# Kernel optimization log

Measured on AMD Instinct MI355X. Metric: run time of the kernel, lower is better.

Reference implementation:

```python
import jax, jax.numpy as jnp
import numpy as np

MAX_DIST = 3          # census patch radius -> 7x7 neighborhood
PATCH = 2 * MAX_DIST + 1


def _warp(img, flow):
    """Bilinear warp (Resample2d): sample img at (x + u, y + v). Coords clamped to border."""
    B, C, H, W = img.shape
    gy, gx = jnp.meshgrid(jnp.arange(H, dtype=img.dtype), jnp.arange(W, dtype=img.dtype), indexing='ij')
    x = gx[None] + flow[:, 0]           # [B,H,W]
    y = gy[None] + flow[:, 1]
    x0 = jnp.floor(x); y0 = jnp.floor(y)
    wx = x - x0; wy = y - y0            # bilinear weights
    x0i = jnp.clip(x0, 0, W - 1).astype(jnp.int32)
    x1i = jnp.clip(x0 + 1.0, 0, W - 1).astype(jnp.int32)
    y0i = jnp.clip(y0, 0, H - 1).astype(jnp.int32)
    y1i = jnp.clip(y0 + 1.0, 0, H - 1).astype(jnp.int32)

    def gather(im_b, yi, xi):           # im_b [C,H,W], yi/xi [H,W] -> [C,H,W]
        return im_b[:, yi, xi]
    g = jax.vmap(gather)
    Ia = g(img, y0i, x0i); Ib = g(img, y0i, x1i)
    Ic = g(img, y1i, x0i); Id = g(img, y1i, x1i)
    wx = wx[:, None]; wy = wy[:, None]  # [B,1,H,W]
    return Ia * (1 - wx) * (1 - wy) + Ib * wx * (1 - wy) + Ic * (1 - wx) * wy + Id * wx * wy


def _census_transform(image):
    """Ternary census transform: grayscale, extract 7x7 patches, normalized center differences."""
    gray = (0.299 * image[:, 0:1] + 0.587 * image[:, 1:2] + 0.114 * image[:, 2:3]) * 255.0
    w = jnp.eye(PATCH * PATCH, dtype=image.dtype).reshape(PATCH * PATCH, 1, PATCH, PATCH)
    patches = jax.lax.conv_general_dilated(
        gray, w, window_strides=(1, 1), padding=[(MAX_DIST, MAX_DIST)] * 2,
        dimension_numbers=('NCHW', 'OIHW', 'NCHW'))   # [B,49,H,W]
    t = patches - gray
    return t / jnp.sqrt(0.81 + t * t)


def _border_mask(B, H, W, dtype):
    m = jnp.zeros((H, W), dtype).at[MAX_DIST:H - MAX_DIST, MAX_DIST:W - MAX_DIST].set(1.0)
    return jnp.broadcast_to(m[None, None], (B, 1, H, W))


def _charbonnier(x, mask, alpha=0.45, eps=0.001):
    err = (x * x + eps * eps) ** alpha * mask
    return jnp.sum(err) / x.size


def _census_loss(im1, im2_warped, mask):
    t1 = _census_transform(im1)
    t2 = _census_transform(im2_warped)
    d = (t1 - t2) ** 2
    dist = jnp.sum(d / (0.1 + d), axis=1, keepdims=True)   # soft Hamming distance [B,1,H,W]
    B, _, H, W = dist.shape
    return _charbonnier(dist, mask * _border_mask(B, H, W, dist.dtype))


def setup_inputs() -> dict:
    key = jax.random.key(0)
    ks = jax.random.split(key, 6)
    B, H, W = 4, 320, 768
    return {
        'former': jax.random.uniform(ks[0], (B, 3, H, W), jnp.float32),
        'latter': jax.random.uniform(ks[1], (B, 3, H, W), jnp.float32),
        'disp_est_scale': jax.random.normal(ks[2], (B, 2, H, W), jnp.float32) * 3.0,
        'disp_est_scale_2': jax.random.normal(ks[3], (B, 2, H, W), jnp.float32) * 3.0,
        'fw_mask': jax.random.uniform(ks[4], (B, 1, H, W), jnp.float32),
        'bw_mask': jax.random.uniform(ks[5], (B, 1, H, W), jnp.float32),
    }


def reference(former, latter, disp_est_scale, disp_est_scale_2, fw_mask, bw_mask):
    left_est = _warp(latter, disp_est_scale)
    image_loss = _census_loss(former, left_est, fw_mask)
    right_est = _warp(former, disp_est_scale_2)
    image_loss_2 = _census_loss(latter, right_est, bw_mask)
    return (image_loss, image_loss_2)
```

## Files before the change

kernel.cpp:

```cpp
#include <hip/hip_runtime.h>

#define BB 4
#define H 320
#define W 768
#define P (H*W)
#define NPIX (BB*P)

#define TX 32
#define TY 8
#define TW (TX+6)
#define TH (TY+6)
#define HALO (TW*TH)
#define NBX (W/TX)
#define NBY (H/TY)
#define NBLK (NBX*NBY*BB)

__global__ void gray_kernel(const float* __restrict__ former,
                            const float* __restrict__ latter,
                            float* __restrict__ gf, float* __restrict__ gl) {
    int idx = blockIdx.x * blockDim.x + threadIdx.x;
    if (idx >= NPIX) return;
    int b = idx / P;
    int r = idx - b * P;
    const float* f = former + (size_t)b * 3 * P + r;
    const float* l = latter + (size_t)b * 3 * P + r;
    gf[idx] = (0.299f * f[0] + 0.587f * f[P] + 0.114f * f[2 * P]) * 255.f;
    gl[idx] = (0.299f * l[0] + 0.587f * l[P] + 0.114f * l[2 * P]) * 255.f;
}

__device__ __forceinline__ float bilinear(const float* __restrict__ img, float fx, float fy) {
    float x0 = floorf(fx), y0 = floorf(fy);
    float wx = fx - x0, wy = fy - y0;
    float x0c = fminf(fmaxf(x0,       0.f), (float)(W - 1));
    float x1c = fminf(fmaxf(x0 + 1.f, 0.f), (float)(W - 1));
    float y0c = fminf(fmaxf(y0,       0.f), (float)(H - 1));
    float y1c = fminf(fmaxf(y0 + 1.f, 0.f), (float)(H - 1));
    int x0i = (int)x0c, x1i = (int)x1c, y0i = (int)y0c, y1i = (int)y1c;
    float Ia = img[y0i * W + x0i], Ib = img[y0i * W + x1i];
    float Ic = img[y1i * W + x0i], Id = img[y1i * W + x1i];
    float omx = 1.f - wx, omy = 1.f - wy;
    return Ia * omx * omy + Ib * wx * omy + Ic * omx * wy + Id * wx * wy;
}

__global__ __launch_bounds__(256)
void fused_kernel(const float* __restrict__ gf, const float* __restrict__ gl,
                  const float* __restrict__ flow1, const float* __restrict__ flow2,
                  const float* __restrict__ fw_mask, const float* __restrict__ bw_mask,
                  float* __restrict__ partials) {
    __shared__ float sA[HALO], sB[HALO], sC[HALO], sD[HALO];
    const int b   = blockIdx.z;
    const int tx0 = blockIdx.x * TX;
    const int ty0 = blockIdx.y * TY;
    const int tid = threadIdx.x;

    const float* pGF = gf + (size_t)b * P;
    const float* pGL = gl + (size_t)b * P;
    const float* pF1 = flow1 + (size_t)b * 2 * P;
    const float* pF2 = flow2 + (size_t)b * 2 * P;

    for (int i = tid; i < HALO; i += 256) {
        int ly = i / TW, lx = i - ly * TW;
        int gx = min(max(tx0 - 3 + lx, 0), W - 1);
        int gy = min(max(ty0 - 3 + ly, 0), H - 1);
        int o = gy * W + gx;
        sA[i] = pGF[o];
        sC[i] = pGL[o];
        float u1 = pF1[o], v1 = pF1[P + o];
        float u2 = pF2[o], v2 = pF2[P + o];
        sB[i] = bilinear(pGL, (float)gx + u1, (float)gy + v1);
        sD[i] = bilinear(pGF, (float)gx + u2, (float)gy + v2);
    }
    __syncthreads();

    const int lx = tid & 31, ly = tid >> 5;
    const int x = tx0 + lx, y = ty0 + ly;
    float sum1 = 0.f, sum2 = 0.f;

    if (x >= 3 && x < W - 3 && y >= 3 && y < H - 3) {
        const int c = (ly + 3) * TW + (lx + 3);
        const float c1 = sA[c], c2 = sB[c], c3 = sC[c], c4 = sD[c];
        float dist1 = 0.f, dist2 = 0.f;
#pragma unroll
        for (int dy = 0; dy < 7; ++dy) {
            const int ro = (ly + dy) * TW + lx;
            float a[7], bv[7], cv[7], dv[7];
#pragma unroll
            for (int dx = 0; dx < 7; ++dx) { a[dx] = sA[ro + dx]; bv[dx] = sB[ro + dx]; }
#pragma unroll
            for (int dx = 0; dx < 7; ++dx) { cv[dx] = sC[ro + dx]; dv[dx] = sD[ro + dx]; }
#pragma unroll
            for (int dx = 0; dx < 7; ++dx) {
                float t1 = a[dx] - c1;
                float t2 = bv[dx] - c2;
                t1 *= __builtin_amdgcn_rsqf(0.81f + t1 * t1);
                t2 *= __builtin_amdgcn_rsqf(0.81f + t2 * t2);
                float d = t1 - t2; d *= d;
                dist1 += d * __builtin_amdgcn_rcpf(0.1f + d);
            }
#pragma unroll
            for (int dx = 0; dx < 7; ++dx) {
                float t3 = cv[dx] - c3;
                float t4 = dv[dx] - c4;
                t3 *= __builtin_amdgcn_rsqf(0.81f + t3 * t3);
                t4 *= __builtin_amdgcn_rsqf(0.81f + t4 * t4);
                float d = t3 - t4; d *= d;
                dist2 += d * __builtin_amdgcn_rcpf(0.1f + d);
            }
        }
        const float m1 = fw_mask[(size_t)b * P + y * W + x];
        const float m2 = bw_mask[(size_t)b * P + y * W + x];
        sum1 = exp2f(0.45f * log2f(dist1 * dist1 + 1e-6f)) * m1;
        sum2 = exp2f(0.45f * log2f(dist2 * dist2 + 1e-6f)) * m2;
    }

#pragma unroll
    for (int off = 32; off; off >>= 1) {
        sum1 += __shfl_down(sum1, off, 64);
        sum2 += __shfl_down(sum2, off, 64);
    }
    __shared__ float red[8];
    const int wave = tid >> 6, lane = tid & 63;
    if (lane == 0) { red[wave] = sum1; red[4 + wave] = sum2; }
    __syncthreads();
    if (tid == 0) {
        const int blk = (blockIdx.z * NBY + blockIdx.y) * NBX + blockIdx.x;
        partials[2 * blk]     = red[0] + red[1] + red[2] + red[3];
        partials[2 * blk + 1] = red[4] + red[5] + red[6] + red[7];
    }
}

__global__ __launch_bounds__(256)
void reduce_kernel(const float* __restrict__ partials, float* __restrict__ out) {
    const int tid = threadIdx.x;
    float s1 = 0.f, s2 = 0.f;
    for (int i = tid; i < NBLK; i += 256) {
        s1 += partials[2 * i];
        s2 += partials[2 * i + 1];
    }
#pragma unroll
    for (int off = 32; off; off >>= 1) {
        s1 += __shfl_down(s1, off, 64);
        s2 += __shfl_down(s2, off, 64);
    }
    __shared__ float red[8];
    const int wave = tid >> 6, lane = tid & 63;
    if (lane == 0) { red[wave] = s1; red[4 + wave] = s2; }
    __syncthreads();
    if (tid == 0) {
        out[0] = (red[0] + red[1] + red[2] + red[3]) * (1.0f / NPIX);
        out[1] = (red[4] + red[5] + red[6] + red[7]) * (1.0f / NPIX);
    }
}

extern "C" void kernel_launch(void* const* d_in, const int* in_sizes, int n_in,
                              void* d_out, int out_size, void* d_ws, size_t ws_size,
                              hipStream_t stream) {
    (void)in_sizes; (void)n_in; (void)out_size; (void)ws_size;
    const float* former  = (const float*)d_in[0];
    const float* latter  = (const float*)d_in[1];
    const float* flow1   = (const float*)d_in[2];
    const float* flow2   = (const float*)d_in[3];
    const float* fw_mask = (const float*)d_in[4];
    const float* bw_mask = (const float*)d_in[5];
    float* out = (float*)d_out;
    float* ws  = (float*)d_ws;
    float* gf       = ws;
    float* gl       = ws + NPIX;
    float* partials = ws + 2 * (size_t)NPIX;

    gray_kernel<<<(NPIX + 255) / 256, 256, 0, stream>>>(former, latter, gf, gl);
    fused_kernel<<<dim3(NBX, NBY, BB), 256, 0, stream>>>(gf, gl, flow1, flow2,
                                                         fw_mask, bw_mask, partials);
    reduce_kernel<<<1, 256, 0, stream>>>(partials, out);
}
```

Before: 141.3 us.

## Interleave halo planes into float4 LDS array and vectorize census math with float2

Merges the four separate shared-memory halo planes into one float4-per-pixel array, so each neighbor takes one 128-bit LDS read instead of four scalar reads. The arithmetic is rewritten on float2 vectors to encourage packed FP32 instructions, the center tap is skipped because its contribution is zero, and the accumulation is split into two chains to shorten dependency latency. The risk is LDS bank conflicts from the wide reads and a larger shared footprint per block.

```diff
diff --git a/kernel.cpp b/kernel.cpp
--- a/kernel.cpp
+++ b/kernel.cpp
@@ -14,6 +14,9 @@
 #define NBX (W/TX)
 #define NBY (H/TY)
 #define NBLK (NBX*NBY*BB)
+
+typedef float f2 __attribute__((ext_vector_type(2)));
+typedef float f4 __attribute__((ext_vector_type(4)));
 
 __global__ void gray_kernel(const float* __restrict__ former,
                             const float* __restrict__ latter,
@@ -47,7 +50,7 @@
                   const float* __restrict__ flow1, const float* __restrict__ flow2,
                   const float* __restrict__ fw_mask, const float* __restrict__ bw_mask,
                   float* __restrict__ partials) {
-    __shared__ float sA[HALO], sB[HALO], sC[HALO], sD[HALO];
+    __shared__ f4 sT[HALO];
     const int b   = blockIdx.z;
     const int tx0 = blockIdx.x * TX;
     const int ty0 = blockIdx.y * TY;
@@ -63,12 +66,13 @@
         int gx = min(max(tx0 - 3 + lx, 0), W - 1);
         int gy = min(max(ty0 - 3 + ly, 0), H - 1);
         int o = gy * W + gx;
-        sA[i] = pGF[o];
-        sC[i] = pGL[o];
+        float A = pGF[o];
+        float C = pGL[o];
         float u1 = pF1[o], v1 = pF1[P + o];
         float u2 = pF2[o], v2 = pF2[P + o];
-        sB[i] = bilinear(pGL, (float)gx + u1, (float)gy + v1);
-        sD[i] = bilinear(pGF, (float)gx + u2, (float)gy + v2);
+        float Bv = bilinear(pGL, (float)gx + u1, (float)gy + v1);
+        float D  = bilinear(pGF, (float)gx + u2, (float)gy + v2);
+        sT[i] = (f4){A, Bv, C, D};
     }
     __syncthreads();
 
@@ -78,39 +82,38 @@
 
     if (x >= 3 && x < W - 3 && y >= 3 && y < H - 3) {
         const int c = (ly + 3) * TW + (lx + 3);
-        const float c1 = sA[c], c2 = sB[c], c3 = sC[c], c4 = sD[c];
-        float dist1 = 0.f, dist2 = 0.f;
+        const f4 cv = sT[c];
+        const f2 cc1 = cv.lo;
+        const f2 cc2 = cv.hi;
+        f2 distA = {0.f, 0.f};
+        f2 distB = {0.f, 0.f};
 #pragma unroll
         for (int dy = 0; dy < 7; ++dy) {
             const int ro = (ly + dy) * TW + lx;
-            float a[7], bv[7], cv[7], dv[7];
-#pragma unroll
-            for (int dx = 0; dx < 7; ++dx) { a[dx] = sA[ro + dx]; bv[dx] = sB[ro + dx]; }
-#pragma unroll
-            for (int dx = 0; dx < 7; ++dx) { cv[dx] = sC[ro + dx]; dv[dx] = sD[ro + dx]; }
 #pragma unroll
             for (int dx = 0; dx < 7; ++dx) {
-                float t1 = a[dx] - c1;
-                float t2 = bv[dx] - c2;
-                t1 *= __builtin_amdgcn_rsqf(0.81f + t1 * t1);
-                t2 *= __builtin_amdgcn_rsqf(0.81f + t2 * t2);
-                float d = t1 - t2; d *= d;
-                dist1 += d * __builtin_amdgcn_rcpf(0.1f + d);
-            }
-#pragma unroll
-            for (int dx = 0; dx < 7; ++dx) {
-                float t3 = cv[dx] - c3;
-                float t4 = dv[dx] - c4;
-                t3 *= __builtin_amdgcn_rsqf(0.81f + t3 * t3);
-                t4 *= __builtin_amdgcn_rsqf(0.81f + t4 * t4);
-                float d = t3 - t4; d *= d;
-                dist2 += d * __builtin_amdgcn_rcpf(0.1f + d);
+                if (dy == 3 && dx == 3) continue;
+                const f4 n = sT[ro + dx];
+                f2 u = n.lo - cc1;
+                f2 v = n.hi - cc2;
+                const f2 qu = u * u + 0.81f;
+                const f2 qv = v * v + 0.81f;
+                u *= (f2){__builtin_amdgcn_rsqf(qu.x), __builtin_amdgcn_rsqf(qu.y)};
+                v *= (f2){__builtin_amdgcn_rsqf(qv.x), __builtin_amdgcn_rsqf(qv.y)};
+                f2 d = {u.x - u.y, v.x - v.y};
+                d *= d;
+                const f2 den = d + 0.1f;
+                const f2 rr = {__builtin_amdgcn_rcpf(den.x), __builtin_amdgcn_rcpf(den.y)};
+                if (((dy * 7 + dx) & 1) == 0) distA += d * rr;
+                else                          distB += d * rr;
             }
         }
+        const f2 dist = distA + distB;
         const float m1 = fw_mask[(size_t)b * P + y * W + x];
         const float m2 = bw_mask[(size_t)b * P + y * W + x];
-        sum1 = exp2f(0.45f * log2f(dist1 * dist1 + 1e-6f)) * m1;
-        sum2 = exp2f(0.45f * log2f(dist2 * dist2 + 1e-6f)) * m2;
+        const f2 cq = dist * dist + 1e-6f;
+        sum1 = exp2f(0.45f * log2f(cq.x)) * m1;
+        sum2 = exp2f(0.45f * log2f(cq.y)) * m2;
     }
 
 #pragma unroll
```

Result: no change. 138.5 us (-1.9%).
